# Optimization experiments

Measured on AMD Instinct MI355X. Metric: run time of the kernel, lower is better.

The kernel has to match this reference:

```python
import jax, jax.numpy as jnp
import numpy as np

E = 512   # embed_dim
H = 8     # num_heads
D = E // H  # head_dim


def setup_inputs() -> dict:
    key = jax.random.key(0)
    ks = jax.random.split(key, 13)
    B, Nq, Nk = 4, 2048, 2048
    query = jax.random.normal(ks[0], (B, Nq, E), dtype=jnp.float32)
    key_t = jax.random.normal(ks[1], (B, Nk, E), dtype=jnp.float32)
    value = jax.random.normal(ks[2], (B, Nk, E), dtype=jnp.float32)
    geometry_mask = jax.random.bernoulli(ks[3], 0.5, (B, Nq, Nk))  # True = keep
    s = 1.0 / np.sqrt(E)
    Wq = jax.random.normal(ks[4], (E, E), dtype=jnp.float32) * s
    bq = jax.random.normal(ks[5], (E,), dtype=jnp.float32) * 0.01
    Wk = jax.random.normal(ks[6], (E, E), dtype=jnp.float32) * s
    bk = jax.random.normal(ks[7], (E,), dtype=jnp.float32) * 0.01
    Wv = jax.random.normal(ks[8], (E, E), dtype=jnp.float32) * s
    bv = jax.random.normal(ks[9], (E,), dtype=jnp.float32) * 0.01
    Wo = jax.random.normal(ks[10], (E, E), dtype=jnp.float32) * s
    bo = jax.random.normal(ks[11], (E,), dtype=jnp.float32) * 0.01
    return {"query": query, "key": key_t, "value": value,
            "geometry_mask": geometry_mask,
            "Wq": Wq, "bq": bq, "Wk": Wk, "bk": bk,
            "Wv": Wv, "bv": bv, "Wo": Wo, "bo": bo}


def reference(query, key, value, geometry_mask, Wq, bq, Wk, bk, Wv, bv, Wo, bo):
    B, Nq, _ = query.shape
    Nk = key.shape[1]
    scale = D ** -0.5
    # projections -> (B, H, N, D)
    Q = (query @ Wq + bq).reshape(B, Nq, H, D).transpose(0, 2, 1, 3)
    K = (key @ Wk + bk).reshape(B, Nk, H, D).transpose(0, 2, 1, 3)
    V = (value @ Wv + bv).reshape(B, Nk, H, D).transpose(0, 2, 1, 3)
    scores = jnp.einsum('bhqd,bhkd->bhqk', Q, K) * scale
    mask = geometry_mask[:, None, :, :]  # (B,1,Nq,Nk), True = keep
    scores = jnp.where(mask, scores, -jnp.inf)
    attn = jax.nn.softmax(scores, axis=-1)  # dropout p=0 (eval)
    out = jnp.einsum('bhqk,bhkd->bhqd', attn, V)
    out = out.transpose(0, 2, 1, 3).reshape(B, Nq, E)
    return out @ Wo + bo
```

## Files before the change

kernel.cpp:

```cpp
#include <hip/hip_runtime.h>
#include <stdint.h>


typedef __attribute__((ext_vector_type(8))) short bf16x8;
typedef __attribute__((ext_vector_type(4))) float f32x4;

#define SCLQ 0.18033688011112042f

static __device__ __forceinline__ unsigned short f2bf(float f) {
    union { float f; unsigned u; } x; x.f = f;
    unsigned r = x.u + 0x7fffu + ((x.u >> 16) & 1u);
    return (unsigned short)(r >> 16);
}

static __device__ __forceinline__ f32x4 mfma16(bf16x8 a, bf16x8 b, f32x4 c) {
    return __builtin_amdgcn_mfma_f32_16x16x32_bf16(a, b, c, 0, 0, 0);
}

#define GLOAD_LDS16(g, l)                                                            \
    __builtin_amdgcn_global_load_lds((const __attribute__((address_space(1))) void*)(g), \
                                     (__attribute__((address_space(3))) void*)(l), 16, 0, 0)

__global__ __launch_bounds__(256) void prep_kernel(
    const float* __restrict__ q, const float* __restrict__ k, const float* __restrict__ v,
    const int* __restrict__ gm,
    const float* __restrict__ Wq, const float* __restrict__ Wk,
    const float* __restrict__ Wv, const float* __restrict__ Wo,
    short* __restrict__ Xq, short* __restrict__ Xk, short* __restrict__ Xv,
    short* __restrict__ WqT, short* __restrict__ WkT,
    short* __restrict__ WvT, short* __restrict__ WoT,
    unsigned long long* __restrict__ mp)
{
    int bx = blockIdx.x;
    if (bx < 12288) {
        int z = bx >> 12;
        const float* src = (z == 0) ? q : (z == 1) ? k : v;
        short* dst = (z == 0) ? Xq : (z == 1) ? Xk : Xv;
        size_t i = (size_t)(bx & 4095) * 256 + threadIdx.x;
        float4 vv = ((const float4*)src)[i];
        short4 o;
        o.x = (short)f2bf(vv.x); o.y = (short)f2bf(vv.y);
        o.z = (short)f2bf(vv.z); o.w = (short)f2bf(vv.w);
        ((short4*)dst)[i] = o;
    } else if (bx < 12800) {
        int b2 = bx - 12288;
        int z = b2 >> 7;
        const float* W = (z == 0) ? Wq : (z == 1) ? Wk : (z == 2) ? Wv : Wo;
        short* WT = (z == 0) ? WqT : (z == 1) ? WkT : (z == 2) ? WvT : WoT;
        int t = (b2 & 127) * 256 + threadIdx.x;
        int n = t & 511;
        int k0 = (t >> 9) * 8;
        union { short s[8]; int4 v4; } u;
#pragma unroll
        for (int j = 0; j < 8; ++j) u.s[j] = (short)f2bf(W[(size_t)(k0 + j) * 512 + n]);
        *(int4*)(WT + (size_t)n * 512 + k0) = u.v4;
    } else {
        int b3 = bx - 12800;
        int lane = threadIdx.x & 63;
        int row = b3 * 4 + (threadIdx.x >> 6);
        const int* mrow = gm + (size_t)row * 2048;
#pragma unroll 4
        for (int w = 0; w < 32; ++w) {
            unsigned long long bits = __ballot(mrow[w * 64 + lane] != 0);
            if (lane == 0) mp[(size_t)row * 32 + w] = bits;
        }
    }
}

static __device__ __forceinline__ void gemm_body(
    const short* __restrict__ A, const short* __restrict__ BT,
    const float* __restrict__ bias, void* __restrict__ Cout, int mode,
    char* lds, int bx, int by)
{
    const int tid = threadIdx.x;
    const int lane = tid & 63;
    const int wid = tid >> 6;
    const int l15 = lane & 15, l4 = lane >> 4;
    const int m0 = by * 64;
    const int n0 = bx * 128;
    const int wr = wid >> 1, wc = wid & 1;

    f32x4 zero = {0.f, 0.f, 0.f, 0.f};
    f32x4 acc[2][4];
#pragma unroll
    for (int i = 0; i < 2; ++i)
#pragma unroll
        for (int j = 0; j < 4; ++j) acc[i][j] = zero;

    char* Alds = lds;
    char* Blds = lds + 8192;

    for (int t = 0; t < 8; ++t) {
        const int k0 = t * 64;
#pragma unroll
        for (int s = 0; s < 2; ++s) {
            int p = s * 256 + tid;
            int r = p >> 3, c = p & 7;
            GLOAD_LDS16(A + (size_t)(m0 + r) * 512 + k0 + 8 * (c ^ (r & 7)),
                        Alds + s * 4096 + wid * 1024);
        }
#pragma unroll
        for (int s = 0; s < 4; ++s) {
            int p = s * 256 + tid;
            int r = p >> 3, c = p & 7;
            GLOAD_LDS16(BT + (size_t)(n0 + r) * 512 + k0 + 8 * (c ^ (r & 7)),
                        Blds + s * 4096 + wid * 1024);
        }
        __syncthreads();
#pragma unroll
        for (int ks = 0; ks < 2; ++ks) {
            bf16x8 af[2], bfr[4];
#pragma unroll
            for (int mb = 0; mb < 2; ++mb) {
                int row = wr * 32 + mb * 16 + l15;
                af[mb] = *(const bf16x8*)(Alds + row * 128 +
                                          ((ks * 64 + l4 * 16) ^ ((row & 7) << 4)));
            }
#pragma unroll
            for (int nb = 0; nb < 4; ++nb) {
                int row = wc * 64 + nb * 16 + l15;
                bfr[nb] = *(const bf16x8*)(Blds + row * 128 +
                                           ((ks * 64 + l4 * 16) ^ ((row & 7) << 4)));
            }
#pragma unroll
            for (int mb = 0; mb < 2; ++mb)
#pragma unroll
                for (int nb = 0; nb < 4; ++nb)
                    acc[mb][nb] = mfma16(af[mb], bfr[nb], acc[mb][nb]);
        }
        __syncthreads();
    }

#pragma unroll
    for (int nb = 0; nb < 4; ++nb) {
        int n = n0 + wc * 64 + nb * 16 + l15;
        float bv = bias[n];
#pragma unroll
        for (int mb = 0; mb < 2; ++mb) {
#pragma unroll
            for (int r = 0; r < 4; ++r) {
                int m = m0 + wr * 32 + mb * 16 + l4 * 4 + r;
                float val = acc[mb][nb][r] + bv;
                if (mode == 0) val *= SCLQ;
                if (mode == 3) {
                    ((float*)Cout)[(size_t)m * 512 + n] = val;
                } else {
                    int b = m >> 11, tok = m & 2047;
                    int h = n >> 6, d = n & 63;
                    short* o = (short*)Cout;
                    if (mode == 2)
                        o[((size_t)(b * 8 + h) * 64 + d) * 2048 + tok] = (short)f2bf(val);
                    else
                        o[((size_t)(b * 8 + h) * 2048 + tok) * 64 + d] = (short)f2bf(val);
                }
            }
        }
    }
}

__global__ __launch_bounds__(256) void gemm_qkv_kernel(
    const short* __restrict__ Xq, const short* __restrict__ Xk, const short* __restrict__ Xv,
    const short* __restrict__ WqT, const short* __restrict__ WkT, const short* __restrict__ WvT,
    const float* __restrict__ bq, const float* __restrict__ bk, const float* __restrict__ bv,
    short* __restrict__ Qw, short* __restrict__ Kw, short* __restrict__ VTw)
{
    __shared__ char lds[24576];
    int z = blockIdx.z;
    const short* A = (z == 0) ? Xq : (z == 1) ? Xk : Xv;
    const short* BT = (z == 0) ? WqT : (z == 1) ? WkT : WvT;
    const float* bias = (z == 0) ? bq : (z == 1) ? bk : bv;
    void* Cout = (z == 0) ? (void*)Qw : (z == 1) ? (void*)Kw : (void*)VTw;
    gemm_body(A, BT, bias, Cout, z, lds, blockIdx.x, blockIdx.y);
}

__global__ __launch_bounds__(256) void gemm_kernel(
    const short* __restrict__ A, const short* __restrict__ BT,
    const float* __restrict__ bias, void* __restrict__ Cout, int mode)
{
    __shared__ char lds[24576];
    gemm_body(A, BT, bias, Cout, mode, lds, blockIdx.x, blockIdx.y);
}

__global__ __launch_bounds__(512) void attn_kernel(
    const short* __restrict__ Q, const short* __restrict__ K,
    const short* __restrict__ VT, const unsigned long long* __restrict__ mp,
    short* __restrict__ AO)
{
    __shared__ char lds[65536];
    const int tid = threadIdx.x;
    const int lane = tid & 63;
    const int wid = tid >> 6;
    const int l15 = lane & 15, l4 = lane >> 4;
    const int lid = blockIdx.x;
    const int xcd = lid & 7, jj = lid >> 3;
    const int bhi = (xcd << 2) | (jj >> 4);
    const int b = bhi >> 3, h = bhi & 7;
    const int q0 = (jj & 15) * 128 + wid * 16;
    const short* Qp = Q + ((size_t)bhi * 2048 + q0) * 64;
    const short* Kp = K + (size_t)bhi * 2048 * 64;
    const short* Vp = VT + (size_t)bhi * 64 * 2048;

    const int krow = tid >> 3;
    const int kgo  = 8 * ((tid & 7) ^ (krow & 7));
    const int vrow0 = tid >> 4;
    const int vgo   = 8 * ((tid & 15) ^ (vrow0 & 7));
    const int vrow1 = 32 + vrow0;
    const int swl = l15 & 7;

#define STAGE(KT, BUF)                                                               \
    {                                                                                \
        const short* Kn = Kp + (size_t)(KT) * 128 * 64;                              \
        char* Kd = lds + (BUF) * 16384;                                              \
        GLOAD_LDS16(Kn + (size_t)krow * 64 + kgo, Kd + wid * 1024);                  \
        GLOAD_LDS16(Kn + (size_t)(64 + krow) * 64 + kgo, Kd + 8192 + wid * 1024);    \
        const short* Vn = Vp + (KT) * 128;                                           \
        char* Vd = lds + 32768 + (BUF) * 16384;                                      \
        GLOAD_LDS16(Vn + (size_t)vrow0 * 2048 + vgo, Vd + wid * 1024);               \
        GLOAD_LDS16(Vn + (size_t)vrow1 * 2048 + vgo, Vd + 8192 + wid * 1024);        \
    }

    bf16x8 qb[2];
#pragma unroll
    for (int dc = 0; dc < 2; ++dc)
        qb[dc] = *(const bf16x8*)(Qp + l15 * 64 + dc * 32 + l4 * 8);

    f32x4 o[4];
#pragma unroll
    for (int dt = 0; dt < 4; ++dt) o[dt] = f32x4{0.f, 0.f, 0.f, 0.f};
    float mrun = 0.f, lrun = 0.f;

    const unsigned long long* mr0 = mp + ((size_t)b * 2048 + q0 + l15) * 32;

    STAGE(0, 0)
    ulonglong2 mwv = *(const ulonglong2*)(mr0);
    __syncthreads();

#define HALF(H, MW)                                                                  \
    {                                                                                \
        bf16x8 ka[4][2];                                                             \
        _Pragma("unroll") for (int tb = 0; tb < 4; ++tb)                             \
            _Pragma("unroll") for (int dc = 0; dc < 2; ++dc)                         \
                ka[tb][dc] = *(const bf16x8*)(Kc + (H) * 8192 +                      \
                                              (tb * 16 + l15) * 128 +                \
                                              16 * ((dc * 4 + l4) ^ swl));           \
        bf16x8 vb[4][2];                                                             \
        _Pragma("unroll") for (int dt = 0; dt < 4; ++dt)                             \
            _Pragma("unroll") for (int kb = 0; kb < 2; ++kb) {                       \
                const char* vr = Vc + (dt * 16 + l15) * 256;                         \
                uint2 x = *(const uint2*)(vr +                                       \
                    16 * (((H) * 8 + kb * 4 + (l4 >> 1)) ^ swl) + (l4 & 1) * 8);     \
                uint2 y = *(const uint2*)(vr +                                       \
                    16 * (((H) * 8 + kb * 4 + 2 + (l4 >> 1)) ^ swl) + (l4 & 1) * 8); \
                uint4 t; t.x = x.x; t.y = x.y; t.z = y.x; t.w = y.y;                 \
                vb[dt][kb] = *(bf16x8*)&t;                                           \
            }                                                                        \
        const float nm = -mrun;                                                      \
        unsigned long long u64 = (MW) >> (l4 * 4);                                   \
        unsigned ulo = (unsigned)u64, uhi = (unsigned)(u64 >> 32);                   \
        f32x4 sv[4];                                                                 \
        _Pragma("unroll") for (int tb = 0; tb < 4; ++tb) {                           \
            unsigned us = (tb & 2) ? uhi : ulo;                                      \
            f32x4 i0;                                                                \
            _Pragma("unroll") for (int r = 0; r < 4; ++r)                            \
                i0[r] = (us & (1u << (((tb & 1) << 4) + r))) ? nm : -1e30f;          \
            sv[tb] = mfma16(ka[tb][1], qb[1], mfma16(ka[tb][0], qb[0], i0));         \
        }                                                                            \
        float pml;                                                                   \
        {                                                                            \
            f32x4 m0v;                                                               \
            _Pragma("unroll") for (int r = 0; r < 4; ++r)                            \
                m0v[r] = fmaxf(fmaxf(sv[0][r], sv[1][r]), fmaxf(sv[2][r], sv[3][r]));\
            pml = fmaxf(fmaxf(m0v[0], m0v[1]), fmaxf(m0v[2], m0v[3]));               \
        }                                                                            \
        if (__any(pml > 8.f)) {                                                      \
            float pm = fmaxf(pml, __shfl_xor(pml, 16, 64));                          \
            pm = fmaxf(pm, __shfl_xor(pm, 32, 64));                                  \
            float dm = fmaxf(pm, 0.f);                                               \
            float al = exp2f(-dm);                                                   \
            mrun += dm;                                                              \
            lrun *= al;                                                              \
            _Pragma("unroll") for (int r = 0; r < 4; ++r) {                          \
                float alr = __shfl(al, l4 * 4 + r, 64);                              \
                _Pragma("unroll") for (int dt = 0; dt < 4; ++dt) o[dt][r] *= alr;    \
            }                                                                        \
            _Pragma("unroll") for (int tb = 0; tb < 4; ++tb)                         \
                _Pragma("unroll") for (int r = 0; r < 4; ++r) sv[tb][r] -= dm;       \
        }                                                                            \
        _Pragma("unroll") for (int tb = 0; tb < 4; ++tb)                             \
            _Pragma("unroll") for (int r = 0; r < 4; ++r)                            \
                sv[tb][r] = exp2f(sv[tb][r]);                                        \
        {                                                                            \
            f32x4 t0 = (sv[0] + sv[1]) + (sv[2] + sv[3]);                            \
            lrun += (t0[0] + t0[1]) + (t0[2] + t0[3]);                               \
        }                                                                            \
        bf16x8 pa[2];                                                                \
        {                                                                            \
            uint4 t_;                                                                \
            asm("v_cvt_pk_bf16_f32 %0, %1, %2" : "=v"(t_.x) : "v"(sv[0][0]), "v"(sv[0][1])); \
            asm("v_cvt_pk_bf16_f32 %0, %1, %2" : "=v"(t_.y) : "v"(sv[0][2]), "v"(sv[0][3])); \
            asm("v_cvt_pk_bf16_f32 %0, %1, %2" : "=v"(t_.z) : "v"(sv[1][0]), "v"(sv[1][1])); \
            asm("v_cvt_pk_bf16_f32 %0, %1, %2" : "=v"(t_.w) : "v"(sv[1][2]), "v"(sv[1][3])); \
            pa[0] = *(bf16x8*)&t_;                                                   \
            asm("v_cvt_pk_bf16_f32 %0, %1, %2" : "=v"(t_.x) : "v"(sv[2][0]), "v"(sv[2][1])); \
            asm("v_cvt_pk_bf16_f32 %0, %1, %2" : "=v"(t_.y) : "v"(sv[2][2]), "v"(sv[2][3])); \
            asm("v_cvt_pk_bf16_f32 %0, %1, %2" : "=v"(t_.z) : "v"(sv[3][0]), "v"(sv[3][1])); \
            asm("v_cvt_pk_bf16_f32 %0, %1, %2" : "=v"(t_.w) : "v"(sv[3][2]), "v"(sv[3][3])); \
            pa[1] = *(bf16x8*)&t_;                                                   \
        }                                                                            \
        _Pragma("unroll") for (int dt = 0; dt < 4; ++dt)                             \
            o[dt] = mfma16(pa[1], vb[dt][1], mfma16(pa[0], vb[dt][0], o[dt]));       \
    }

    for (int kt = 0; kt < 16; ++kt) {
        const int cur = kt & 1;
        char* Kc = lds + cur * 16384;
        char* Vc = lds + 32768 + cur * 16384;
        if (kt < 15) STAGE(kt + 1, cur ^ 1)
        ulonglong2 mwn;
        mwn.x = 0; mwn.y = 0;
        if (kt < 15) mwn = *(const ulonglong2*)(mr0 + 2 * kt + 2);
        HALF(0, mwv.x)
        HALF(1, mwv.y)
        mwv = mwn;
        __syncthreads();
    }
#undef HALF
#undef STAGE

    {
        float lt = lrun;
        lt += __shfl_xor(lt, 16, 64);
        lt += __shfl_xor(lt, 32, 64);
        float inv = 1.0f / lt;
#pragma unroll
        for (int r = 0; r < 4; ++r) {
            float invr = __shfl(inv, l4 * 4 + r, 64);
            size_t base = ((size_t)b * 2048 + q0 + l4 * 4 + r) * 512 + h * 64;
#pragma unroll
            for (int dt = 0; dt < 4; ++dt)
                AO[base + dt * 16 + l15] = (short)f2bf(o[dt][r] * invr);
        }
    }
}

extern "C" void kernel_launch(void* const* d_in, const int* in_sizes, int n_in,
                              void* d_out, int out_size, void* d_ws, size_t ws_size,
                              hipStream_t stream) {
    const float* q  = (const float*)d_in[0];
    const float* k  = (const float*)d_in[1];
    const float* v  = (const float*)d_in[2];
    const int*   gm = (const int*)d_in[3];
    const float* Wq = (const float*)d_in[4];  const float* bq = (const float*)d_in[5];
    const float* Wk = (const float*)d_in[6];  const float* bk = (const float*)d_in[7];
    const float* Wv = (const float*)d_in[8];  const float* bv = (const float*)d_in[9];
    const float* Wo = (const float*)d_in[10]; const float* bo = (const float*)d_in[11];

    char* ws = (char*)d_ws;
    short* Xq  = (short*)(ws + 0);
    short* Xk  = (short*)(ws + 8388608);
    short* Xv  = (short*)(ws + 16777216);
    short* WqT = (short*)(ws + 25165824);
    short* WkT = (short*)(ws + 25690112);
    short* WvT = (short*)(ws + 26214400);
    short* WoT = (short*)(ws + 26738688);
    short* Qw  = (short*)(ws + 27262976);
    short* Kw  = (short*)(ws + 35651584);
    short* VTw = (short*)(ws + 44040192);
    short* AO  = (short*)(ws + 52428800);
    unsigned long long* MP = (unsigned long long*)(ws + 60817408);

    prep_kernel<<<dim3(14848), 256, 0, stream>>>(q, k, v, gm, Wq, Wk, Wv, Wo,
                                                 Xq, Xk, Xv, WqT, WkT, WvT, WoT, MP);

    gemm_qkv_kernel<<<dim3(4, 128, 3), 256, 0, stream>>>(Xq, Xk, Xv, WqT, WkT, WvT,
                                                         bq, bk, bv, Qw, Kw, VTw);

    attn_kernel<<<dim3(512), 512, 0, stream>>>(Qw, Kw, VTw, MP, AO);

    gemm_kernel<<<dim3(4, 128), 256, 0, stream>>>(AO, WoT, bo, (void*)d_out, 3);
}
```

Before: 159.8 us.

## Fuse fp32-to-bf16 input conversion into QKV GEMM and move mask packing there

The separate pass that converts q/k/v from fp32 to bf16 in workspace is removed. The QKV GEMM now loads fp32 A tiles directly, converts them with v_cvt_pk_bf16_f32 and writes them into swizzled LDS. Mask bit-packing moves into an extra z-slice of the QKV GEMM grid, so the prep kernel only transposes the weights. This avoids writing and re-reading 24 MB of bf16 intermediates. In exchange the A loads become synchronous register loads instead of async global_load_lds, and each A tile is re-read as fp32 by every N-block (4x).

```diff
diff --git a/kernel.cpp b/kernel.cpp
--- a/kernel.cpp
+++ b/kernel.cpp
@@ -21,54 +21,26 @@
     __builtin_amdgcn_global_load_lds((const __attribute__((address_space(1))) void*)(g), \
                                      (__attribute__((address_space(3))) void*)(l), 16, 0, 0)
 
-__global__ __launch_bounds__(256) void prep_kernel(
-    const float* __restrict__ q, const float* __restrict__ k, const float* __restrict__ v,
-    const int* __restrict__ gm,
+__global__ __launch_bounds__(256) void prep_w_kernel(
     const float* __restrict__ Wq, const float* __restrict__ Wk,
     const float* __restrict__ Wv, const float* __restrict__ Wo,
-    short* __restrict__ Xq, short* __restrict__ Xk, short* __restrict__ Xv,
     short* __restrict__ WqT, short* __restrict__ WkT,
-    short* __restrict__ WvT, short* __restrict__ WoT,
-    unsigned long long* __restrict__ mp)
-{
-    int bx = blockIdx.x;
-    if (bx < 12288) {
-        int z = bx >> 12;
-        const float* src = (z == 0) ? q : (z == 1) ? k : v;
-        short* dst = (z == 0) ? Xq : (z == 1) ? Xk : Xv;
-        size_t i = (size_t)(bx & 4095) * 256 + threadIdx.x;
-        float4 vv = ((const float4*)src)[i];
-        short4 o;
-        o.x = (short)f2bf(vv.x); o.y = (short)f2bf(vv.y);
-        o.z = (short)f2bf(vv.z); o.w = (short)f2bf(vv.w);
-        ((short4*)dst)[i] = o;
-    } else if (bx < 12800) {
-        int b2 = bx - 12288;
-        int z = b2 >> 7;
-        const float* W = (z == 0) ? Wq : (z == 1) ? Wk : (z == 2) ? Wv : Wo;
-        short* WT = (z == 0) ? WqT : (z == 1) ? WkT : (z == 2) ? WvT : WoT;
-        int t = (b2 & 127) * 256 + threadIdx.x;
-        int n = t & 511;
-        int k0 = (t >> 9) * 8;
-        union { short s[8]; int4 v4; } u;
-#pragma unroll
-        for (int j = 0; j < 8; ++j) u.s[j] = (short)f2bf(W[(size_t)(k0 + j) * 512 + n]);
-        *(int4*)(WT + (size_t)n * 512 + k0) = u.v4;
-    } else {
-        int b3 = bx - 12800;
-        int lane = threadIdx.x & 63;
-        int row = b3 * 4 + (threadIdx.x >> 6);
-        const int* mrow = gm + (size_t)row * 2048;
-#pragma unroll 4
-        for (int w = 0; w < 32; ++w) {
-            unsigned long long bits = __ballot(mrow[w * 64 + lane] != 0);
-            if (lane == 0) mp[(size_t)row * 32 + w] = bits;
-        }
-    }
+    short* __restrict__ WvT, short* __restrict__ WoT)
+{
+    int z = blockIdx.x >> 7;
+    const float* W = (z == 0) ? Wq : (z == 1) ? Wk : (z == 2) ? Wv : Wo;
+    short* WT = (z == 0) ? WqT : (z == 1) ? WkT : (z == 2) ? WvT : WoT;
+    int t = (blockIdx.x & 127) * 256 + threadIdx.x;
+    int n = t & 511;
+    int k0 = (t >> 9) * 8;
+    union { short s[8]; int4 v4; } u;
+#pragma unroll
+    for (int j = 0; j < 8; ++j) u.s[j] = (short)f2bf(W[(size_t)(k0 + j) * 512 + n]);
+    *(int4*)(WT + (size_t)n * 512 + k0) = u.v4;
 }
 
 static __device__ __forceinline__ void gemm_body(
-    const short* __restrict__ A, const short* __restrict__ BT,
+    const void* __restrict__ Avoid, int a_f32, const short* __restrict__ BT,
     const float* __restrict__ bias, void* __restrict__ Cout, int mode,
     char* lds, int bx, int by)
 {
@@ -92,12 +64,31 @@
 
     for (int t = 0; t < 8; ++t) {
         const int k0 = t * 64;
-#pragma unroll
-        for (int s = 0; s < 2; ++s) {
-            int p = s * 256 + tid;
-            int r = p >> 3, c = p & 7;
-            GLOAD_LDS16(A + (size_t)(m0 + r) * 512 + k0 + 8 * (c ^ (r & 7)),
-                        Alds + s * 4096 + wid * 1024);
+        if (a_f32) {
+            const float* A32 = (const float*)Avoid;
+#pragma unroll
+            for (int s = 0; s < 2; ++s) {
+                int p = s * 256 + tid;
+                int r = p >> 3, c = p & 7;
+                const float* src = A32 + (size_t)(m0 + r) * 512 + k0 + 8 * c;
+                float4 f0 = *(const float4*)(src);
+                float4 f1 = *(const float4*)(src + 4);
+                uint4 w;
+                asm("v_cvt_pk_bf16_f32 %0, %1, %2" : "=v"(w.x) : "v"(f0.x), "v"(f0.y));
+                asm("v_cvt_pk_bf16_f32 %0, %1, %2" : "=v"(w.y) : "v"(f0.z), "v"(f0.w));
+                asm("v_cvt_pk_bf16_f32 %0, %1, %2" : "=v"(w.z) : "v"(f1.x), "v"(f1.y));
+                asm("v_cvt_pk_bf16_f32 %0, %1, %2" : "=v"(w.w) : "v"(f1.z), "v"(f1.w));
+                *(uint4*)(Alds + r * 128 + 16 * (c ^ (r & 7))) = w;
+            }
+        } else {
+            const short* A16 = (const short*)Avoid;
+#pragma unroll
+            for (int s = 0; s < 2; ++s) {
+                int p = s * 256 + tid;
+                int r = p >> 3, c = p & 7;
+                GLOAD_LDS16(A16 + (size_t)(m0 + r) * 512 + k0 + 8 * (c ^ (r & 7)),
+                            Alds + s * 4096 + wid * 1024);
+            }
         }
 #pragma unroll
         for (int s = 0; s < 4; ++s) {
@@ -159,18 +150,35 @@
 }
 
 __global__ __launch_bounds__(256) void gemm_qkv_kernel(
-    const short* __restrict__ Xq, const short* __restrict__ Xk, const short* __restrict__ Xv,
+    const float* __restrict__ q, const float* __restrict__ k, const float* __restrict__ v,
     const short* __restrict__ WqT, const short* __restrict__ WkT, const short* __restrict__ WvT,
     const float* __restrict__ bq, const float* __restrict__ bk, const float* __restrict__ bv,
-    short* __restrict__ Qw, short* __restrict__ Kw, short* __restrict__ VTw)
+    short* __restrict__ Qw, short* __restrict__ Kw, short* __restrict__ VTw,
+    const int* __restrict__ gm, unsigned long long* __restrict__ mp)
 {
     __shared__ char lds[24576];
     int z = blockIdx.z;
-    const short* A = (z == 0) ? Xq : (z == 1) ? Xk : Xv;
+    if (z == 3) {
+        int bid = blockIdx.y * 4 + blockIdx.x;
+        int lane = threadIdx.x & 63;
+        int wv = threadIdx.x >> 6;
+#pragma unroll
+        for (int p = 0; p < 4; ++p) {
+            int row = bid * 16 + p * 4 + wv;
+            const int* mrow = gm + (size_t)row * 2048;
+#pragma unroll 4
+            for (int w = 0; w < 32; ++w) {
+                unsigned long long bits = __ballot(mrow[w * 64 + lane] != 0);
+                if (lane == 0) mp[(size_t)row * 32 + w] = bits;
+            }
+        }
+        return;
+    }
+    const float* A = (z == 0) ? q : (z == 1) ? k : v;
     const short* BT = (z == 0) ? WqT : (z == 1) ? WkT : WvT;
     const float* bias = (z == 0) ? bq : (z == 1) ? bk : bv;
     void* Cout = (z == 0) ? (void*)Qw : (z == 1) ? (void*)Kw : (void*)VTw;
-    gemm_body(A, BT, bias, Cout, z, lds, blockIdx.x, blockIdx.y);
+    gemm_body(A, 1, BT, bias, Cout, z, lds, blockIdx.x, blockIdx.y);
 }
 
 __global__ __launch_bounds__(256) void gemm_kernel(
@@ -178,7 +186,7 @@
     const float* __restrict__ bias, void* __restrict__ Cout, int mode)
 {
     __shared__ char lds[24576];
-    gemm_body(A, BT, bias, Cout, mode, lds, blockIdx.x, blockIdx.y);
+    gemm_body(A, 0, BT, bias, Cout, mode, lds, blockIdx.x, blockIdx.y);
 }
 
 __global__ __launch_bounds__(512) void attn_kernel(
@@ -356,9 +364,6 @@
     const float* Wo = (const float*)d_in[10]; const float* bo = (const float*)d_in[11];
 
     char* ws = (char*)d_ws;
-    short* Xq  = (short*)(ws + 0);
-    short* Xk  = (short*)(ws + 8388608);
-    short* Xv  = (short*)(ws + 16777216);
     short* WqT = (short*)(ws + 25165824);
     short* WkT = (short*)(ws + 25690112);
     short* WvT = (short*)(ws + 26214400);
@@ -369,11 +374,11 @@
     short* AO  = (short*)(ws + 52428800);
     unsigned long long* MP = (unsigned long long*)(ws + 60817408);
 
-    prep_kernel<<<dim3(14848), 256, 0, stream>>>(q, k, v, gm, Wq, Wk, Wv, Wo,
-                                                 Xq, Xk, Xv, WqT, WkT, WvT, WoT, MP);
-
-    gemm_qkv_kernel<<<dim3(4, 128, 3), 256, 0, stream>>>(Xq, Xk, Xv, WqT, WkT, WvT,
-                                                         bq, bk, bv, Qw, Kw, VTw);
+    prep_w_kernel<<<dim3(512), 256, 0, stream>>>(Wq, Wk, Wv, Wo, WqT, WkT, WvT, WoT);
+
+    gemm_qkv_kernel<<<dim3(4, 128, 4), 256, 0, stream>>>(q, k, v, WqT, WkT, WvT,
+                                                         bq, bk, bv, Qw, Kw, VTw,
+                                                         gm, MP);
 
     attn_kernel<<<dim3(512), 512, 0, stream>>>(Qw, Kw, VTw, MP, AO);
 
```

New measurement: 173.3 us. 8.5% more time.
